# Performance work log

Hardware: AMD Instinct MI355X
Metric: run time of the kernel (lower is better)

The kernel has to match this reference:

```python
import jax, jax.numpy as jnp
import numpy as np

BATCH = 10000
NUM_TREES = 1000
NUM_NODES = 511  # full binary tree of depth 8
N_FEATURES = 256
N_CLASSES = 1
MAX_DEPTH = 8


def setup_inputs() -> dict:
    key = jax.random.key(0)
    k = jax.random.split(key, 6)
    flat = NUM_TREES * NUM_NODES
    x = jax.random.normal(k[0], (BATCH, N_FEATURES), dtype=jnp.float32)
    thresholds = jax.random.normal(k[1], (flat,), dtype=jnp.float32)
    values = jax.random.normal(k[2], (flat, N_CLASSES), dtype=jnp.float32)
    lefts = jax.random.randint(k[3], (flat,), 0, NUM_NODES).astype(jnp.int64)
    rights = jax.random.randint(k[4], (flat,), 0, NUM_NODES).astype(jnp.int64)
    features = jax.random.randint(k[5], (flat,), 0, N_FEATURES).astype(jnp.int64)
    return {
        "x": x,
        "thresholds": thresholds,
        "values": values,
        "lefts": lefts,
        "rights": rights,
        "features": features,
        "num_trees": NUM_TREES,
        "num_nodes": NUM_NODES,
        "max_depth": MAX_DEPTH,
    }


def reference(x, thresholds, values, lefts, rights, features, num_trees, num_nodes, max_depth):
    batch = x.shape[0]
    # nodes_offset: flat index of each tree's root in the concatenated node arrays
    nodes_offset = (jnp.arange(num_trees, dtype=jnp.int32) * num_nodes)[None, :]  # [1, T]
    indexes = jnp.broadcast_to(nodes_offset, (batch, num_trees))  # [B, T]
    for _ in range(max_depth):
        feature_nodes = features[indexes]                     # [B, T] feature id per current node
        feature_values = jnp.take_along_axis(x, feature_nodes, axis=1)  # [B, T]
        thr = thresholds[indexes]                             # [B, T]
        l = lefts[indexes]                                    # [B, T]
        r = rights[indexes]                                   # [B, T]
        indexes = jnp.where(feature_values >= thr, r, l) + nodes_offset
    output = values[indexes]  # [B, T, C]
    return output
```

## Files before the change

### kernel.cpp

```cpp
#include <hip/hip_runtime.h>
#include <stdint.h>

#define BATCH     10000
#define NUM_TREES 1000
#define NUM_NODES 511
#define NFEAT     256
#define DEPTH     8
#define FLAT_NODES (NUM_TREES * NUM_NODES)

#define TREE_BYTES 1360
#define VLEAF_OFF  ((size_t)NUM_TREES * TREE_BYTES)
#define WS_NEEDED  (VLEAF_OFF + (size_t)NUM_TREES * 256 * 4)
#define XT_LD      10048
#define XT_OFF     WS_NEEDED
#define XT_BYTES   ((size_t)NFEAT * XT_LD * 4)
#define WS_XT      (XT_OFF + XT_BYTES)

#define BT 64
#define TT 64
#define NTHREADS 1024
#define XS_BYTES  (NFEAT * 64 * 4)
#define OUT_LD    36
#define OS_BYTES  (64 * OUT_LD * 4)
#define SH_BYTES  (XS_BYTES + OS_BYTES)

__device__ __forceinline__ void glds16(const void* g, void* l) {
  __builtin_amdgcn_global_load_lds(
      (const __attribute__((address_space(1))) unsigned int*)g,
      (__attribute__((address_space(3))) unsigned int*)l, 16, 0, 0);
}

__global__ __launch_bounds__(256)
void unroll_kernel(const float* __restrict__ thr,
                   const int* __restrict__ feats,
                   const int* __restrict__ lefts,
                   const int* __restrict__ rights,
                   const float* __restrict__ values,
                   unsigned char* __restrict__ ws) {
  __shared__ uint16_t n_s[4][512];
  const int wv = threadIdx.x >> 6, lane = threadIdx.x & 63;
  const int tree = blockIdx.x * 4 + wv;
  const int base = tree * NUM_NODES;
  uint16_t* n = n_s[wv];
  uint4* rec   = (uint4*)(ws + (size_t)tree * TREE_BYTES);
  float* vleaf = (float*)(ws + VLEAF_OFF + (size_t)tree * 1024);

  if (lane == 0) n[0] = 0;
  __syncthreads();
  const int EBASE[4] = {0, 1, 5, 21};
  #pragma unroll
  for (int d = 0; d < 8; ++d) {
    const int lvl = (1 << d) - 1, cnt = 1 << d;
    for (int i = lane; i < cnt; i += 64) {
      int p  = lvl + i;
      int np = n[p];
      int nl = lefts[base + np], nr = rights[base + np];
      n[2 * p + 1] = (uint16_t)nl;
      n[2 * p + 2] = (uint16_t)nr;
      if ((d & 1) == 0) {
        uint32_t f3 = (uint32_t)feats[base + np] |
                      ((uint32_t)feats[base + nl] << 8) |
                      ((uint32_t)feats[base + nr] << 16);
        rec[EBASE[d >> 1] + i] =
            make_uint4(__float_as_uint(thr[base + np]),
                       __float_as_uint(thr[base + nl]),
                       __float_as_uint(thr[base + nr]), f3);
      }
    }
    __syncthreads();
  }
  #pragma unroll
  for (int i = lane; i < 256; i += 64)
    vleaf[i] = values[base + n[255 + i]];
}

__global__ __launch_bounds__(256)
void transpose_kernel(const float* __restrict__ x, float* __restrict__ xT) {
  __shared__ float tile[64][65];
  const int tid = threadIdx.x;
  const int b0 = blockIdx.x * 64, f0 = blockIdx.y * 64;
  const float4* xg = (const float4*)x;
  #pragma unroll
  for (int p = 0; p < 4; ++p) {
    int i = tid + p * 256;
    int r = i >> 4, c4 = i & 15;
    int gb = b0 + r;
    float4 v = (gb < BATCH) ? xg[(size_t)gb * 64 + (f0 >> 2) + c4]
                            : make_float4(0.f, 0.f, 0.f, 0.f);
    tile[r][4 * c4 + 0] = v.x;
    tile[r][4 * c4 + 1] = v.y;
    tile[r][4 * c4 + 2] = v.z;
    tile[r][4 * c4 + 3] = v.w;
  }
  __syncthreads();
  #pragma unroll
  for (int p = 0; p < 4; ++p) {
    int i = tid + p * 256;
    int fr = i >> 4, b4 = i & 15;
    float4 w = make_float4(tile[4 * b4 + 0][fr], tile[4 * b4 + 1][fr],
                           tile[4 * b4 + 2][fr], tile[4 * b4 + 3][fr]);
    *(float4*)(xT + (size_t)(f0 + fr) * XT_LD + b0 + 4 * b4) = w;
  }
}

template <bool XT>
__global__ __launch_bounds__(NTHREADS, 8)
void traverse64(const float* __restrict__ x,
                const unsigned char* __restrict__ ws,
                float* __restrict__ out) {
  extern __shared__ unsigned char smem[];
  float* x_s   = (float*)smem;
  float* out_s = (float*)(smem + XS_BYTES);

  const int tid  = threadIdx.x;
  const int wid  = tid >> 6;
  const int lane = tid & 63;
  const int b0   = blockIdx.y * BT;
  const int t0   = blockIdx.x * TT;

  if (XT) {
    const float* xT = (const float*)(ws + XT_OFF);
    #pragma unroll
    for (int k = 0; k < 4; ++k) {
      int fi = tid + k * NTHREADS;
      int f = fi >> 4, c16 = fi & 15;
      glds16(xT + (size_t)f * XT_LD + b0 + 4 * c16,
             (unsigned char*)x_s + (size_t)fi * 16);
    }
  } else {
    const float4* xg = (const float4*)x;
    #pragma unroll
    for (int p = 0; p < 4; ++p) {
      int i = tid + p * NTHREADS;
      int r = i >> 6, c = i & 63;
      int gb = b0 + r;
      float4 v = (gb < BATCH) ? xg[(size_t)gb * 64 + c]
                              : make_float4(0.f, 0.f, 0.f, 0.f);
      int o = (c << 8) + (r ^ (c & 31));
      x_s[o]       = v.x;
      x_s[o + 64]  = v.y;
      x_s[o + 128] = v.z;
      x_s[o + 192] = v.w;
    }
  }
  __syncthreads();

  auto xgather = [&](int f) -> float {
    if (XT) return x_s[(f << 6) + lane];
    return x_s[(f << 6) + (lane ^ ((f >> 2) & 31))];
  };

  const unsigned char* nb = ws + (size_t)(t0 + 4 * wid) * TREE_BYTES;
  int loc[4] = {0, 0, 0, 0};
  #pragma unroll
  for (int it = 0; it < 4; ++it) {
    const int eoff = (it == 0) ? 0 : (it == 1) ? 16 : (it == 2) ? 80 : 336;
    uint4 r[4];
    #pragma unroll
    for (int c = 0; c < 4; ++c)
      r[c] = *(const uint4*)(nb + (size_t)c * TREE_BYTES + loc[c] * 16 + eoff);
    float xp[4];
    #pragma unroll
    for (int c = 0; c < 4; ++c)
      xp[c] = xgather(r[c].w & 255);
    bool  c0[4]; int fc[4]; float tc[4];
    #pragma unroll
    for (int c = 0; c < 4; ++c) {
      c0[c] = (xp[c] >= __uint_as_float(r[c].x));
      fc[c] = c0[c] ? ((r[c].w >> 16) & 255) : ((r[c].w >> 8) & 255);
      tc[c] = __uint_as_float(c0[c] ? r[c].z : r[c].y);
    }
    float xc[4];
    #pragma unroll
    for (int c = 0; c < 4; ++c)
      xc[c] = xgather(fc[c]);
    #pragma unroll
    for (int c = 0; c < 4; ++c)
      loc[c] = 4 * loc[c] + 2 * (int)c0[c] + (int)(xc[c] >= tc[c]);
  }
  const float* vl = (const float*)(ws + VLEAF_OFF);
  float4 v;
  {
    const int gt0 = t0 + 4 * wid;
    int g0 = (gt0 + 0 < NUM_TREES) ? gt0 + 0 : 0;
    int g1 = (gt0 + 1 < NUM_TREES) ? gt0 + 1 : 0;
    int g2 = (gt0 + 2 < NUM_TREES) ? gt0 + 2 : 0;
    int g3 = (gt0 + 3 < NUM_TREES) ? gt0 + 3 : 0;
    v = make_float4(vl[(size_t)g0 * 256 + loc[0]],
                    vl[(size_t)g1 * 256 + loc[1]],
                    vl[(size_t)g2 * 256 + loc[2]],
                    vl[(size_t)g3 * 256 + loc[3]]);
  }

  if (wid < 8)
    *(float4*)(out_s + lane * OUT_LD + 4 * wid) = v;
  __syncthreads();
  {
    int col = tid & 31, rr = tid >> 5;
    #pragma unroll
    for (int k = 0; k < 2; ++k) {
      int row = rr + 32 * k;
      int gb = b0 + row, gt = t0 + col;
      if (gb < BATCH && gt < NUM_TREES)
        out[(size_t)gb * NUM_TREES + gt] = out_s[row * OUT_LD + col];
    }
  }
  __syncthreads();
  if (wid >= 8)
    *(float4*)(out_s + lane * OUT_LD + 4 * (wid - 8)) = v;
  __syncthreads();
  {
    int col = tid & 31, rr = tid >> 5;
    #pragma unroll
    for (int k = 0; k < 2; ++k) {
      int row = rr + 32 * k;
      int gb = b0 + row, gt = t0 + 32 + col;
      if (gb < BATCH && gt < NUM_TREES)
        out[(size_t)gb * NUM_TREES + gt] = out_s[row * OUT_LD + col];
    }
  }
}

#define FB_BT 64
#define FB_TT 64
#define FB_TPR 16
#define FB_NROUNDS 4
#define FB_NTHREADS 1024
#define FB_XS (NFEAT * 64 * 4)
#define FB_NSU (FB_TPR * NUM_NODES)
#define FB_NS (FB_NSU * 8)
#define FB_OLD (FB_TT + 1)
#define FB_OS (FB_BT * FB_OLD * 4)
#define FB_SH (FB_XS + FB_NS + FB_OS)
#define FB_PREF ((FB_NSU + FB_NTHREADS - 1) / FB_NTHREADS)

__global__ __launch_bounds__(FB_NTHREADS, 1)
void fb_traverse(const float* __restrict__ x,
                 const float* __restrict__ thrg,
                 const int* __restrict__ featg,
                 const int* __restrict__ leftg,
                 const int* __restrict__ rightg,
                 const float* __restrict__ values,
                 float* __restrict__ out) {
  extern __shared__ unsigned char smem[];
  float* x_s     = (float*)smem;
  uint2* nodes_s = (uint2*)(smem + FB_XS);
  float* out_s   = (float*)(smem + FB_XS + FB_NS);
  const int tid = threadIdx.x, wid = tid >> 6, lane = tid & 63;
  const int b0 = blockIdx.y * FB_BT, t0 = blockIdx.x * FB_TT;
  uint2 pf[FB_PREF];
  auto load_round = [&](int rr) {
    const int gbase = (t0 + rr * FB_TPR) * NUM_NODES;
    #pragma unroll
    for (int k = 0; k < FB_PREF; ++k) {
      int fi = tid + k * FB_NTHREADS;
      uint2 v = make_uint2(0u, 0u);
      if (fi < FB_NSU) {
        int gi = gbase + fi;
        if (gi < FLAT_NODES) {
          uint32_t meta = (uint32_t)featg[gi] | ((uint32_t)leftg[gi] << 8) |
                          ((uint32_t)rightg[gi] << 20);
          v = make_uint2(__float_as_uint(thrg[gi]), meta);
        }
      }
      pf[k] = v;
    }
  };
  auto write_nodes = [&]() {
    #pragma unroll
    for (int k = 0; k < FB_PREF; ++k) {
      int fi = tid + k * FB_NTHREADS;
      if (fi < FB_NSU) nodes_s[fi] = pf[k];
    }
  };
  load_round(0);
  {
    const float4* xg = (const float4*)x;
    #pragma unroll
    for (int p = 0; p < (FB_BT * (NFEAT / 4)) / FB_NTHREADS; ++p) {
      int i = tid + p * FB_NTHREADS;
      int r = i >> 6, c = i & 63;
      int gb = b0 + r;
      float4 v = make_float4(0.f, 0.f, 0.f, 0.f);
      if (gb < BATCH) v = xg[gb * (NFEAT / 4) + c];
      int o = (c << 8) + (r ^ (c & 31));
      x_s[o] = v.x; x_s[o + 64] = v.y; x_s[o + 128] = v.z; x_s[o + 192] = v.w;
    }
  }
  write_nodes();
  __syncthreads();
  for (int r = 0; r < FB_NROUNDS; ++r) {
    if (r + 1 < FB_NROUNDS) load_round(r + 1);
    const uint2* nA = nodes_s + wid * NUM_NODES;
    const int tr0 = t0 + r * FB_TPR;
    const int gta = tr0 + wid;
    const int offA = (gta < NUM_TREES ? gta : 0) * NUM_NODES;
    uint2 na = nA[0];
    float va = 0.f;
    #pragma unroll
    for (int d = 0; d < DEPTH; ++d) {
      int fa = na.y & 0xFF;
      int la = (na.y >> 8) & 0xFFF;
      int ra = (int)(na.y >> 20);
      float xa = x_s[(fa << 6) + (lane ^ ((fa >> 2) & 31))];
      if (d < DEPTH - 1) {
        uint2 nla = nA[la], nra = nA[ra];
        na = (xa >= __uint_as_float(na.x)) ? nra : nla;
      } else {
        float vla = values[offA + la], vra = values[offA + ra];
        va = (xa >= __uint_as_float(na.x)) ? vra : vla;
      }
    }
    out_s[lane * FB_OLD + r * FB_TPR + wid] = va;
    __syncthreads();
    if (r + 1 < FB_NROUNDS) { write_nodes(); __syncthreads(); }
  }
  {
    const int gt = t0 + lane;
    #pragma unroll
    for (int p = 0; p < FB_BT / 16; ++p) {
      int rr = p * 16 + wid;
      int gb = b0 + rr;
      if (gb < BATCH && gt < NUM_TREES)
        out[gb * NUM_TREES + gt] = out_s[rr * FB_OLD + lane];
    }
  }
}

extern "C" void kernel_launch(void* const* d_in, const int* in_sizes, int n_in,
                              void* d_out, int out_size, void* d_ws, size_t ws_size,
                              hipStream_t stream) {
  const float* x          = (const float*)d_in[0];
  const float* thresholds = (const float*)d_in[1];
  const float* values     = (const float*)d_in[2];
  const int*   lefts      = (const int*)d_in[3];
  const int*   rights     = (const int*)d_in[4];
  const int*   features   = (const int*)d_in[5];
  float* out = (float*)d_out;

  if (ws_size >= WS_XT) {
    unsigned char* ws = (unsigned char*)d_ws;
    unroll_kernel<<<NUM_TREES / 4, 256, 0, stream>>>(
        thresholds, features, lefts, rights, values, ws);
    transpose_kernel<<<dim3((BATCH + 63) / 64, NFEAT / 64), 256, 0, stream>>>(
        x, (float*)(ws + XT_OFF));
    hipFuncSetAttribute(reinterpret_cast<const void*>(traverse64<true>),
                        hipFuncAttributeMaxDynamicSharedMemorySize, SH_BYTES);
    dim3 grid((NUM_TREES + TT - 1) / TT, (BATCH + BT - 1) / BT);
    traverse64<true><<<grid, NTHREADS, SH_BYTES, stream>>>(x, ws, out);
  } else if (ws_size >= WS_NEEDED) {
    unsigned char* ws = (unsigned char*)d_ws;
    unroll_kernel<<<NUM_TREES / 4, 256, 0, stream>>>(
        thresholds, features, lefts, rights, values, ws);
    hipFuncSetAttribute(reinterpret_cast<const void*>(traverse64<false>),
                        hipFuncAttributeMaxDynamicSharedMemorySize, SH_BYTES);
    dim3 grid((NUM_TREES + TT - 1) / TT, (BATCH + BT - 1) / BT);
    traverse64<false><<<grid, NTHREADS, SH_BYTES, stream>>>(x, ws, out);
  } else {
    hipFuncSetAttribute(reinterpret_cast<const void*>(fb_traverse),
                        hipFuncAttributeMaxDynamicSharedMemorySize, FB_SH);
    dim3 grid((NUM_TREES + FB_TT - 1) / FB_TT, (BATCH + FB_BT - 1) / FB_BT);
    fb_traverse<<<grid, FB_NTHREADS, FB_SH, stream>>>(
        x, thresholds, features, lefts, rights, values, out);
  }
}
```

Measured before the change: 57.97 us.

## Fuse tree unroll and x transpose into one prepack launch; speculate child gathers

Merges the tree-unrolling kernel and the x transpose kernel into a single launch, with each block picking its role from its block index, which removes one kernel launch and its serialization gap. In the traversal kernel, the first node record is loaded before the x tile is staged so its latency overlaps the LDS fill. Each two-level step now gathers both children's feature values up front and selects between them, instead of waiting on the parent comparison before the second gather. This removes a dependent LDS round trip per step at the cost of one extra LDS read per tree per step, and the next record load is issued at the end of each step.

```diff
diff --git a/kernel.cpp b/kernel.cpp
--- a/kernel.cpp
+++ b/kernel.cpp
@@ -24,6 +24,9 @@
 #define OS_BYTES  (64 * OUT_LD * 4)
 #define SH_BYTES  (XS_BYTES + OS_BYTES)
 
+#define UNROLL_BLOCKS 250
+#define TRANS_BLOCKS  (157 * 4)
+
 __device__ __forceinline__ void glds16(const void* g, void* l) {
   __builtin_amdgcn_global_load_lds(
       (const __attribute__((address_space(1))) unsigned int*)g,
@@ -31,75 +34,79 @@
 }
 
 __global__ __launch_bounds__(256)
-void unroll_kernel(const float* __restrict__ thr,
-                   const int* __restrict__ feats,
-                   const int* __restrict__ lefts,
-                   const int* __restrict__ rights,
-                   const float* __restrict__ values,
-                   unsigned char* __restrict__ ws) {
-  __shared__ uint16_t n_s[4][512];
-  const int wv = threadIdx.x >> 6, lane = threadIdx.x & 63;
-  const int tree = blockIdx.x * 4 + wv;
-  const int base = tree * NUM_NODES;
-  uint16_t* n = n_s[wv];
-  uint4* rec   = (uint4*)(ws + (size_t)tree * TREE_BYTES);
-  float* vleaf = (float*)(ws + VLEAF_OFF + (size_t)tree * 1024);
-
-  if (lane == 0) n[0] = 0;
-  __syncthreads();
-  const int EBASE[4] = {0, 1, 5, 21};
-  #pragma unroll
-  for (int d = 0; d < 8; ++d) {
-    const int lvl = (1 << d) - 1, cnt = 1 << d;
-    for (int i = lane; i < cnt; i += 64) {
-      int p  = lvl + i;
-      int np = n[p];
-      int nl = lefts[base + np], nr = rights[base + np];
-      n[2 * p + 1] = (uint16_t)nl;
-      n[2 * p + 2] = (uint16_t)nr;
-      if ((d & 1) == 0) {
-        uint32_t f3 = (uint32_t)feats[base + np] |
-                      ((uint32_t)feats[base + nl] << 8) |
-                      ((uint32_t)feats[base + nr] << 16);
-        rec[EBASE[d >> 1] + i] =
-            make_uint4(__float_as_uint(thr[base + np]),
-                       __float_as_uint(thr[base + nl]),
-                       __float_as_uint(thr[base + nr]), f3);
+void prepack_kernel(const float* __restrict__ thr,
+                    const int* __restrict__ feats,
+                    const int* __restrict__ lefts,
+                    const int* __restrict__ rights,
+                    const float* __restrict__ values,
+                    const float* __restrict__ x,
+                    unsigned char* __restrict__ ws) {
+  __shared__ unsigned char sh[64 * 65 * 4];
+  const int tid = threadIdx.x;
+
+  if (blockIdx.x < UNROLL_BLOCKS) {
+    uint16_t* n_s = (uint16_t*)sh;
+    const int wv = tid >> 6, lane = tid & 63;
+    const int tree = blockIdx.x * 4 + wv;
+    const int base = tree * NUM_NODES;
+    uint16_t* n = n_s + wv * 512;
+    uint4* rec   = (uint4*)(ws + (size_t)tree * TREE_BYTES);
+    float* vleaf = (float*)(ws + VLEAF_OFF + (size_t)tree * 1024);
+
+    if (lane == 0) n[0] = 0;
+    __syncthreads();
+    const int EBASE[4] = {0, 1, 5, 21};
+    #pragma unroll
+    for (int d = 0; d < 8; ++d) {
+      const int lvl = (1 << d) - 1, cnt = 1 << d;
+      for (int i = lane; i < cnt; i += 64) {
+        int p  = lvl + i;
+        int np = n[p];
+        int nl = lefts[base + np], nr = rights[base + np];
+        n[2 * p + 1] = (uint16_t)nl;
+        n[2 * p + 2] = (uint16_t)nr;
+        if ((d & 1) == 0) {
+          uint32_t f3 = (uint32_t)feats[base + np] |
+                        ((uint32_t)feats[base + nl] << 8) |
+                        ((uint32_t)feats[base + nr] << 16);
+          rec[EBASE[d >> 1] + i] =
+              make_uint4(__float_as_uint(thr[base + np]),
+                         __float_as_uint(thr[base + nl]),
+                         __float_as_uint(thr[base + nr]), f3);
+        }
       }
+      __syncthreads();
+    }
+    #pragma unroll
+    for (int i = lane; i < 256; i += 64)
+      vleaf[i] = values[base + n[255 + i]];
+  } else {
+    float (*tile)[65] = (float(*)[65])sh;
+    float* xT = (float*)(ws + XT_OFF);
+    const int t = blockIdx.x - UNROLL_BLOCKS;
+    const int b0 = (t >> 2) * 64, f0 = (t & 3) * 64;
+    const float4* xg = (const float4*)x;
+    #pragma unroll
+    for (int p = 0; p < 4; ++p) {
+      int i = tid + p * 256;
+      int r = i >> 4, c4 = i & 15;
+      int gb = b0 + r;
+      float4 v = (gb < BATCH) ? xg[(size_t)gb * 64 + (f0 >> 2) + c4]
+                              : make_float4(0.f, 0.f, 0.f, 0.f);
+      tile[r][4 * c4 + 0] = v.x;
+      tile[r][4 * c4 + 1] = v.y;
+      tile[r][4 * c4 + 2] = v.z;
+      tile[r][4 * c4 + 3] = v.w;
     }
     __syncthreads();
-  }
-  #pragma unroll
-  for (int i = lane; i < 256; i += 64)
-    vleaf[i] = values[base + n[255 + i]];
-}
-
-__global__ __launch_bounds__(256)
-void transpose_kernel(const float* __restrict__ x, float* __restrict__ xT) {
-  __shared__ float tile[64][65];
-  const int tid = threadIdx.x;
-  const int b0 = blockIdx.x * 64, f0 = blockIdx.y * 64;
-  const float4* xg = (const float4*)x;
-  #pragma unroll
-  for (int p = 0; p < 4; ++p) {
-    int i = tid + p * 256;
-    int r = i >> 4, c4 = i & 15;
-    int gb = b0 + r;
-    float4 v = (gb < BATCH) ? xg[(size_t)gb * 64 + (f0 >> 2) + c4]
-                            : make_float4(0.f, 0.f, 0.f, 0.f);
-    tile[r][4 * c4 + 0] = v.x;
-    tile[r][4 * c4 + 1] = v.y;
-    tile[r][4 * c4 + 2] = v.z;
-    tile[r][4 * c4 + 3] = v.w;
-  }
-  __syncthreads();
-  #pragma unroll
-  for (int p = 0; p < 4; ++p) {
-    int i = tid + p * 256;
-    int fr = i >> 4, b4 = i & 15;
-    float4 w = make_float4(tile[4 * b4 + 0][fr], tile[4 * b4 + 1][fr],
-                           tile[4 * b4 + 2][fr], tile[4 * b4 + 3][fr]);
-    *(float4*)(xT + (size_t)(f0 + fr) * XT_LD + b0 + 4 * b4) = w;
+    #pragma unroll
+    for (int p = 0; p < 4; ++p) {
+      int i = tid + p * 256;
+      int fr = i >> 4, b4 = i & 15;
+      float4 w = make_float4(tile[4 * b4 + 0][fr], tile[4 * b4 + 1][fr],
+                             tile[4 * b4 + 2][fr], tile[4 * b4 + 3][fr]);
+      *(float4*)(xT + (size_t)(f0 + fr) * XT_LD + b0 + 4 * b4) = w;
+    }
   }
 }
 
@@ -118,6 +125,12 @@
   const int b0   = blockIdx.y * BT;
   const int t0   = blockIdx.x * TT;
 
+  const unsigned char* nb = ws + (size_t)(t0 + 4 * wid) * TREE_BYTES;
+  uint4 r[4];
+  #pragma unroll
+  for (int c = 0; c < 4; ++c)
+    r[c] = *(const uint4*)(nb + (size_t)c * TREE_BYTES);
+
   if (XT) {
     const float* xT = (const float*)(ws + XT_OFF);
     #pragma unroll
@@ -132,11 +145,11 @@
     #pragma unroll
     for (int p = 0; p < 4; ++p) {
       int i = tid + p * NTHREADS;
-      int r = i >> 6, c = i & 63;
-      int gb = b0 + r;
+      int rr = i >> 6, c = i & 63;
+      int gb = b0 + rr;
       float4 v = (gb < BATCH) ? xg[(size_t)gb * 64 + c]
                               : make_float4(0.f, 0.f, 0.f, 0.f);
-      int o = (c << 8) + (r ^ (c & 31));
+      int o = (c << 8) + (rr ^ (c & 31));
       x_s[o]       = v.x;
       x_s[o + 64]  = v.y;
       x_s[o + 128] = v.z;
@@ -150,33 +163,29 @@
     return x_s[(f << 6) + (lane ^ ((f >> 2) & 31))];
   };
 
-  const unsigned char* nb = ws + (size_t)(t0 + 4 * wid) * TREE_BYTES;
   int loc[4] = {0, 0, 0, 0};
   #pragma unroll
   for (int it = 0; it < 4; ++it) {
-    const int eoff = (it == 0) ? 0 : (it == 1) ? 16 : (it == 2) ? 80 : 336;
-    uint4 r[4];
-    #pragma unroll
-    for (int c = 0; c < 4; ++c)
-      r[c] = *(const uint4*)(nb + (size_t)c * TREE_BYTES + loc[c] * 16 + eoff);
-    float xp[4];
-    #pragma unroll
-    for (int c = 0; c < 4; ++c)
+    float xp[4], xl[4], xr[4];
+    #pragma unroll
+    for (int c = 0; c < 4; ++c) {
       xp[c] = xgather(r[c].w & 255);
-    bool  c0[4]; int fc[4]; float tc[4];
+      xl[c] = xgather((r[c].w >> 8) & 255);
+      xr[c] = xgather((r[c].w >> 16) & 255);
+    }
     #pragma unroll
     for (int c = 0; c < 4; ++c) {
-      c0[c] = (xp[c] >= __uint_as_float(r[c].x));
-      fc[c] = c0[c] ? ((r[c].w >> 16) & 255) : ((r[c].w >> 8) & 255);
-      tc[c] = __uint_as_float(c0[c] ? r[c].z : r[c].y);
-    }
-    float xc[4];
-    #pragma unroll
-    for (int c = 0; c < 4; ++c)
-      xc[c] = xgather(fc[c]);
-    #pragma unroll
-    for (int c = 0; c < 4; ++c)
-      loc[c] = 4 * loc[c] + 2 * (int)c0[c] + (int)(xc[c] >= tc[c]);
+      bool c0  = (xp[c] >= __uint_as_float(r[c].x));
+      float xc = c0 ? xr[c] : xl[c];
+      float tc = __uint_as_float(c0 ? r[c].z : r[c].y);
+      loc[c] = 4 * loc[c] + 2 * (int)c0 + (int)(xc >= tc);
+    }
+    if (it < 3) {
+      const int eoff = (it == 0) ? 16 : (it == 1) ? 80 : 336;
+      #pragma unroll
+      for (int c = 0; c < 4; ++c)
+        r[c] = *(const uint4*)(nb + (size_t)c * TREE_BYTES + loc[c] * 16 + eoff);
+    }
   }
   const float* vl = (const float*)(ws + VLEAF_OFF);
   float4 v;
@@ -340,18 +349,16 @@
 
   if (ws_size >= WS_XT) {
     unsigned char* ws = (unsigned char*)d_ws;
-    unroll_kernel<<<NUM_TREES / 4, 256, 0, stream>>>(
-        thresholds, features, lefts, rights, values, ws);
-    transpose_kernel<<<dim3((BATCH + 63) / 64, NFEAT / 64), 256, 0, stream>>>(
-        x, (float*)(ws + XT_OFF));
+    prepack_kernel<<<UNROLL_BLOCKS + TRANS_BLOCKS, 256, 0, stream>>>(
+        thresholds, features, lefts, rights, values, x, ws);
     hipFuncSetAttribute(reinterpret_cast<const void*>(traverse64<true>),
                         hipFuncAttributeMaxDynamicSharedMemorySize, SH_BYTES);
     dim3 grid((NUM_TREES + TT - 1) / TT, (BATCH + BT - 1) / BT);
     traverse64<true><<<grid, NTHREADS, SH_BYTES, stream>>>(x, ws, out);
   } else if (ws_size >= WS_NEEDED) {
     unsigned char* ws = (unsigned char*)d_ws;
-    unroll_kernel<<<NUM_TREES / 4, 256, 0, stream>>>(
-        thresholds, features, lefts, rights, values, ws);
+    prepack_kernel<<<UNROLL_BLOCKS, 256, 0, stream>>>(
+        thresholds, features, lefts, rights, values, x, ws);
     hipFuncSetAttribute(reinterpret_cast<const void*>(traverse64<false>),
                         hipFuncAttributeMaxDynamicSharedMemorySize, SH_BYTES);
     dim3 grid((NUM_TREES + TT - 1) / TT, (BATCH + BT - 1) / BT);
```

New measurement: 55.10 us, median of 2. 1.05x faster.
